# Kernel tuning notes

Measured on AMD Instinct MI355X. Metric: run time of the kernel, lower is better.

## Reference

```python
import jax, jax.numpy as jnp
import numpy as np

N = 100000       # nodes
E = 1600000      # edges (before self loops)
D = 128          # emb_dim
L = 5            # num_layer
NBOND = 62       # num_bond_type
NNODE = 2159     # num_node_type + 2
BN_EPS = 1e-5


def setup_inputs() -> dict:
    key = jax.random.key(0)
    ks = jax.random.split(key, 8)
    x = jax.random.randint(ks[0], (N, 1), 0, NNODE)
    edge_index = jax.random.randint(ks[1], (2, E), 0, N)
    edge_attr = jax.random.randint(ks[2], (E, 1), 0, NBOND)
    x_emb = jax.random.normal(ks[3], (NNODE, D), dtype=jnp.float32) * 0.02
    lin_w = jax.random.normal(ks[4], (L, D, D), dtype=jnp.float32) * (1.0 / np.sqrt(D))
    lin_b = jnp.zeros((L, D), jnp.float32)
    edge_tab = jax.random.normal(ks[5], (L, NBOND, D), dtype=jnp.float32) * 0.02
    bn_gamma = jnp.ones((L, D), jnp.float32)
    bn_beta = jnp.zeros((L, D), jnp.float32)
    return {"x": x, "edge_index": edge_index, "edge_attr": edge_attr,
            "x_emb": x_emb, "lin_w": lin_w, "lin_b": lin_b,
            "edge_tab": edge_tab, "bn_gamma": bn_gamma, "bn_beta": bn_beta}


def reference(x, edge_index, edge_attr, x_emb, lin_w, lin_b, edge_tab, bn_gamma, bn_beta):
    # node embedding lookup: x_embedding(x[:, 0])
    h = x_emb[x[:, 0]]                                  # [N, D]

    # add self loops (same for every layer in the torch code)
    loop = jnp.arange(N)
    src = jnp.concatenate([edge_index[0], loop])        # [E+N] = j (source)
    dst = jnp.concatenate([edge_index[1], loop])        # [E+N] = i (target)
    eids = jnp.concatenate([edge_attr[:, 0], jnp.zeros((N,), edge_attr.dtype)])

    # GCN symmetric norm: deg from row (=src), deg_inv_sqrt[row]*deg_inv_sqrt[col]
    deg = jax.ops.segment_sum(jnp.ones(src.shape, h.dtype), src, num_segments=N)
    dinv = jnp.where(deg > 0, jax.lax.rsqrt(deg), jnp.zeros_like(deg))
    norm = (dinv[src] * dinv[dst])[:, None]             # [E+N, 1]

    for l in range(L):
        # linear transform of nodes
        hl = h @ lin_w[l].T + lin_b[l]                  # [N, D]
        # message: norm * (x_j + edge_embedding), gather from source nodes
        msg = norm * (hl[src] + edge_tab[l][eids])      # [E+N, D]
        # aggr='add': scatter_add into target nodes
        agg = jax.ops.segment_sum(msg, dst, num_segments=N)  # [N, D]
        # BatchNorm1d (training-mode batch statistics, biased variance)
        mean = agg.mean(axis=0)
        var = jnp.mean((agg - mean) ** 2, axis=0)
        h = (agg - mean) * jax.lax.rsqrt(var + BN_EPS) * bn_gamma[l] + bn_beta[l]
        if l < L - 1:
            h = jax.nn.relu(h)
        # dropout with drop_ratio=0 is identity
    # JK == 'last'
    return h
```

## Files before the change

### kernel.cpp

```cpp
#include <hip/hip_runtime.h>

#define NN 100000
#define NE 1600000
#define NT (NE + NN)
#define DD 128
#define NL 5
#define NB 62
#define BN_EPS 1e-5f
#define NBUCK 391
#define PSUMNB 6250
#define RED1 128

typedef unsigned short ushort_t;
typedef unsigned int uint_t;
typedef short bf8 __attribute__((ext_vector_type(8)));
typedef float f32x4 __attribute__((ext_vector_type(4)));

static __device__ __forceinline__ float4 ld4(const float* p) { return *(const float4*)p; }

static __device__ __forceinline__ float bfhi(uint_t u) {
    uint_t x = u & 0xFFFF0000u;
    return __builtin_bit_cast(float, x);
}
static __device__ __forceinline__ float bflo(uint_t u) {
    uint_t x = u << 16;
    return __builtin_bit_cast(float, x);
}
static __device__ __forceinline__ ushort_t f2bf(float f) {
    uint_t u = __builtin_bit_cast(uint_t, f);
    u += 0x7FFFu + ((u >> 16) & 1u);
    return (ushort_t)(u >> 16);
}


__global__ void k_init(int* gbh_d, int* gbh_s, float* scale, float* shift,
                       int* row_ptr) {
    int i = blockIdx.x * 256 + threadIdx.x;
    if (i < NBUCK) { gbh_d[i] = 0; gbh_s[i] = 0; }
    if (i < DD) { scale[i] = 1.f; shift[i] = 0.f; }
    if (i == 0) row_ptr[NN] = NT;
}

__global__ void k_cvt(const float* __restrict__ src, ushort_t* __restrict__ dst,
                      int total) {
    int i = blockIdx.x * 256 + threadIdx.x;
    if (i < total) dst[i] = f2bf(src[i]);
}

__global__ __launch_bounds__(256) void k_binhist(const int* __restrict__ ei,
                                                 int* __restrict__ gbh_d,
                                                 int* __restrict__ gbh_s) {
    __shared__ int hd[NBUCK], hs[NBUCK];
    int tid = threadIdx.x;
    for (int b = tid; b < NBUCK; b += 256) { hd[b] = 0; hs[b] = 0; }
    __syncthreads();
    for (int idx = blockIdx.x * 256 + tid; idx < NT; idx += gridDim.x * 256) {
        int d = (idx < NE) ? ei[NE + idx] : idx - NE;
        atomicAdd(&hd[d >> 8], 1);
        if (idx < NE) atomicAdd(&hs[ei[idx] >> 8], 1);
    }
    __syncthreads();
    for (int b = tid; b < NBUCK; b += 256) {
        if (hd[b]) atomicAdd(&gbh_d[b], hd[b]);
        if (hs[b]) atomicAdd(&gbh_s[b], hs[b]);
    }
}

__global__ void k_scan391(const int* __restrict__ gbh_d, const int* __restrict__ gbh_s,
                          int* __restrict__ bb_d, int* __restrict__ cur_d,
                          int* __restrict__ bb_s, int* __restrict__ cur_s) {
    __shared__ int s[512];
    const int* g = blockIdx.x ? gbh_s : gbh_d;
    int* bb = blockIdx.x ? bb_s : bb_d;
    int* cur = blockIdx.x ? cur_s : cur_d;
    int t = threadIdx.x;
    int v = (t < NBUCK) ? g[t] : 0;
    s[t] = v;
    __syncthreads();
    for (int off = 1; off < 512; off <<= 1) {
        int val = (t >= off) ? s[t - off] : 0;
        __syncthreads();
        s[t] += val;
        __syncthreads();
    }
    if (t < NBUCK) { int e = s[t] - v; bb[t] = e; cur[t] = e; }
    if (t == 511) bb[NBUCK] = s[511];
}

#define CHUNK 4096
__global__ __launch_bounds__(256) void k_scat2(const int* __restrict__ ei,
                                               const int* __restrict__ ea,
                                               int* __restrict__ cur_d,
                                               int* __restrict__ cur_s,
                                               uint_t* __restrict__ rec_d,
                                               int* __restrict__ rec_s) {
    __shared__ int lhd[NBUCK], lbd[NBUCK], lhs[NBUCK], lbs[NBUCK];
    int tid = threadIdx.x;
    for (int b = tid; b < NBUCK; b += 256) { lhd[b] = 0; lhs[b] = 0; }
    __syncthreads();
    int base = blockIdx.x * CHUNK;
    uint_t rd[16];
    int rs[16], bkd[16], bks[16];
#pragma unroll
    for (int k = 0; k < 16; ++k) {
        int idx = base + tid + k * 256;
        bkd[k] = -1; bks[k] = -1;
        if (idx < NT) {
            int s, d, eid;
            if (idx < NE) {
                s = ei[idx]; d = ei[NE + idx]; eid = ea[idx];
                bks[k] = s >> 8; rs[k] = s;
                atomicAdd(&lhs[bks[k]], 1);
            } else {
                s = d = idx - NE; eid = 0;
            }
            bkd[k] = d >> 8;
            rd[k] = (uint_t)s | ((uint_t)eid << 17) | ((uint_t)(d & 255) << 24);
            atomicAdd(&lhd[bkd[k]], 1);
        }
    }
    __syncthreads();
    for (int b = tid; b < NBUCK; b += 256) {
        if (lhd[b]) lbd[b] = atomicAdd(&cur_d[b], lhd[b]);
        if (lhs[b]) lbs[b] = atomicAdd(&cur_s[b], lhs[b]);
    }
    __syncthreads();
    for (int b = tid; b < NBUCK; b += 256) { lhd[b] = 0; lhs[b] = 0; }
    __syncthreads();
#pragma unroll
    for (int k = 0; k < 16; ++k) {
        if (bkd[k] >= 0) {
            int rk = atomicAdd(&lhd[bkd[k]], 1);
            rec_d[lbd[bkd[k]] + rk] = rd[k];
        }
        if (bks[k] >= 0) {
            int rk = atomicAdd(&lhs[bks[k]], 1);
            rec_s[lbs[bks[k]] + rk] = rs[k];
        }
    }
}

__global__ __launch_bounds__(256) void k_srcfin(const int* __restrict__ rec,
                                                const int* __restrict__ bb,
                                                float* __restrict__ dinv) {
    __shared__ int h[256];
    int tid = threadIdx.x;
    h[tid] = 0;
    __syncthreads();
    int lo = bb[blockIdx.x], hi = bb[blockIdx.x + 1];
    for (int i = lo + tid; i < hi; i += 256) atomicAdd(&h[rec[i] & 255], 1);
    __syncthreads();
    int v = blockIdx.x * 256 + tid;
    if (v < NN) dinv[v] = rsqrtf((float)(h[tid] + 1));
}

__global__ __launch_bounds__(256) void k_dstfin(const uint_t* __restrict__ rec,
                                                const int* __restrict__ bb,
                                                const float* __restrict__ dinv,
                                                int* __restrict__ row_ptr,
                                                int* __restrict__ s_pack,
                                                float* __restrict__ s_norm) {
    __shared__ int h[256], sc[256], rpE[256];
    int tid = threadIdx.x;
    h[tid] = 0;
    __syncthreads();
    int lo = bb[blockIdx.x], hi = bb[blockIdx.x + 1];
    for (int i = lo + tid; i < hi; i += 256) atomicAdd(&h[(rec[i] >> 24) & 255], 1);
    __syncthreads();
    sc[tid] = h[tid];
    __syncthreads();
    for (int off = 1; off < 256; off <<= 1) {
        int val = (tid >= off) ? sc[tid - off] : 0;
        __syncthreads();
        sc[tid] += val;
        __syncthreads();
    }
    rpE[tid] = sc[tid] - h[tid];
    int v = blockIdx.x * 256 + tid;
    if (v < NN) row_ptr[v] = lo + rpE[tid];
    h[tid] = 0;
    __syncthreads();
    for (int i = lo + tid; i < hi; i += 256) {
        uint_t u = rec[i];
        int dl = (u >> 24) & 255;
        int rk = atomicAdd(&h[dl], 1);
        int slot = lo + rpE[dl] + rk;
        int s = u & 0x1FFFF;
        int e = (u >> 17) & 0x3F;
        s_pack[slot] = s | (e << 20);
        s_norm[slot] = dinv[s] * dinv[(blockIdx.x << 8) + dl];
    }
}

__global__ void k_h0b(const int* __restrict__ x, const float* __restrict__ emb,
                      ushort_t* __restrict__ Xb, int n) {
    int v = blockIdx.x * 16 + (threadIdx.x >> 4);
    if (v >= n) return;
    int c8 = (threadIdx.x & 15) * 8;
    const float* src = &emb[x[v] * DD + c8];
    uint_t pk[4];
#pragma unroll
    for (int j = 0; j < 4; ++j)
        pk[j] = (uint_t)f2bf(src[2 * j]) | ((uint_t)f2bf(src[2 * j + 1]) << 16);
    *(uint4*)&Xb[(size_t)v * DD + c8] = make_uint4(pk[0], pk[1], pk[2], pk[3]);
}


__global__ __launch_bounds__(256, 2) void k_gemm(const ushort_t* __restrict__ Xb,
                                                 const ushort_t* __restrict__ Wb,
                                                 const float* __restrict__ bias,
                                                 const float* __restrict__ scale,
                                                 const float* __restrict__ shift,
                                                 ushort_t* __restrict__ C,
                                                 int n, int relu) {
    __shared__ ushort_t As[128 * DD];
    __shared__ ushort_t Bs[128 * DD];
    const int tid = threadIdx.x;
    const int r0 = blockIdx.x * 128;
    const int rl = tid >> 4;
    const int kg = tid & 15;

    float sc[8], sh[8];
    *(float4*)&sc[0] = ld4(&scale[kg * 8]);
    *(float4*)&sc[4] = ld4(&scale[kg * 8 + 4]);
    *(float4*)&sh[0] = ld4(&shift[kg * 8]);
    *(float4*)&sh[4] = ld4(&shift[kg * 8 + 4]);

#pragma unroll
    for (int it = 0; it < 8; ++it) {
        int row = rl + it * 16;
        int grow = r0 + row;
        uint4 v = make_uint4(0, 0, 0, 0);
        if (grow < n) v = *(const uint4*)&Xb[(size_t)grow * DD + kg * 8];
        uint_t pk[4];
        const uint_t* pv = (const uint_t*)&v;
#pragma unroll
        for (int j = 0; j < 4; ++j) {
            float lo = fmaf(bflo(pv[j]), sc[2 * j], sh[2 * j]);
            float hi = fmaf(bfhi(pv[j]), sc[2 * j + 1], sh[2 * j + 1]);
            if (relu) { lo = fmaxf(lo, 0.f); hi = fmaxf(hi, 0.f); }
            pk[j] = (uint_t)f2bf(lo) | ((uint_t)f2bf(hi) << 16);
        }
        *(uint4*)&As[row * DD + (kg ^ (row & 7)) * 8] = make_uint4(pk[0], pk[1], pk[2], pk[3]);
        uint4 wv = *(const uint4*)&Wb[row * DD + kg * 8];
        *(uint4*)&Bs[row * DD + (kg ^ (row & 7)) * 8] = wv;
    }
    __syncthreads();

    const int w = tid >> 6;
    const int lane = tid & 63;
    const int lr = lane & 15;
    const int lg = lane >> 4;

    f32x4 acc[2][8];
#pragma unroll
    for (int rf = 0; rf < 2; ++rf)
#pragma unroll
        for (int cf = 0; cf < 8; ++cf)
#pragma unroll
            for (int r = 0; r < 4; ++r) acc[rf][cf][r] = 0.f;

#pragma unroll
    for (int ks = 0; ks < 4; ++ks) {
        int kgg = ks * 4 + lg;
        bf8 a0, a1;
        {
            int row = w * 32 + lr;
            a0 = *(bf8*)&As[row * DD + (kgg ^ (row & 7)) * 8];
            row += 16;
            a1 = *(bf8*)&As[row * DD + (kgg ^ (row & 7)) * 8];
        }
#pragma unroll
        for (int cf = 0; cf < 8; ++cf) {
            int col = cf * 16 + lr;
            bf8 b = *(bf8*)&Bs[col * DD + (kgg ^ (col & 7)) * 8];
            acc[0][cf] = __builtin_amdgcn_mfma_f32_16x16x32_bf16(a0, b, acc[0][cf], 0, 0, 0);
            acc[1][cf] = __builtin_amdgcn_mfma_f32_16x16x32_bf16(a1, b, acc[1][cf], 0, 0, 0);
        }
    }

#pragma unroll
    for (int cf = 0; cf < 8; ++cf) {
        int col = cf * 16 + lr;
        float bi = bias[col];
#pragma unroll
        for (int rf = 0; rf < 2; ++rf) {
#pragma unroll
            for (int r = 0; r < 4; ++r) {
                int grow = r0 + w * 32 + rf * 16 + lg * 4 + r;
                if (grow < n) C[(size_t)grow * DD + col] = f2bf(acc[rf][cf][r] + bi);
            }
        }
    }
}

__global__ __launch_bounds__(1024) void k_agg(const ushort_t* __restrict__ hl,
                                              const ushort_t* __restrict__ etab,
                                              const int* __restrict__ row_ptr,
                                              const int* __restrict__ s_pack,
                                              const float* __restrict__ s_norm,
                                              ushort_t* __restrict__ aggb,
                                              float* __restrict__ psumA,
                                              float* __restrict__ psumB, int n) {
    __shared__ float lsA[16][DD], lsB[16][DD];
    int tid = threadIdx.x;
    int wv = tid >> 6;
    int lane = tid & 63;
    int g = lane >> 4;
    int fl = lane & 15;
    int lane8 = fl * 8;
    int v = blockIdx.x * 16 + wv;
    int p0 = row_ptr[v], p1 = row_ptr[v + 1];

    float acc[8];
#pragma unroll
    for (int j = 0; j < 8; ++j) acc[j] = 0.f;
    for (int p = p0 + g; p < p1; p += 4) {
        int c = s_pack[p];
        float nr = s_norm[p];
        int s = c & 0xFFFFF;
        int e = c >> 20;
        uint4 hv = *(const uint4*)&hl[(size_t)s * DD + lane8];
        uint4 ev = *(const uint4*)&etab[e * DD + lane8];
        acc[0] = fmaf(nr, bflo(hv.x) + bflo(ev.x), acc[0]);
        acc[1] = fmaf(nr, bfhi(hv.x) + bfhi(ev.x), acc[1]);
        acc[2] = fmaf(nr, bflo(hv.y) + bflo(ev.y), acc[2]);
        acc[3] = fmaf(nr, bfhi(hv.y) + bfhi(ev.y), acc[3]);
        acc[4] = fmaf(nr, bflo(hv.z) + bflo(ev.z), acc[4]);
        acc[5] = fmaf(nr, bfhi(hv.z) + bfhi(ev.z), acc[5]);
        acc[6] = fmaf(nr, bflo(hv.w) + bflo(ev.w), acc[6]);
        acc[7] = fmaf(nr, bfhi(hv.w) + bfhi(ev.w), acc[7]);
    }
#pragma unroll
    for (int j = 0; j < 8; ++j) {
        acc[j] += __shfl_xor(acc[j], 16);
        acc[j] += __shfl_xor(acc[j], 32);
    }
    if (g == 0) {
        uint_t pk[4];
#pragma unroll
        for (int j = 0; j < 4; ++j)
            pk[j] = (uint_t)f2bf(acc[2 * j]) | ((uint_t)f2bf(acc[2 * j + 1]) << 16);
        *(uint4*)&aggb[(size_t)v * DD + lane8] = make_uint4(pk[0], pk[1], pk[2], pk[3]);
#pragma unroll
        for (int j = 0; j < 8; ++j) {
            lsA[wv][lane8 + j] = acc[j];
            lsB[wv][lane8 + j] = acc[j] * acc[j];
        }
    }
    __syncthreads();
    if (tid < DD) {
        float a = 0.f, b = 0.f;
#pragma unroll
        for (int k = 0; k < 16; ++k) { a += lsA[k][tid]; b += lsB[k][tid]; }
        psumA[(size_t)blockIdx.x * DD + tid] = a;
        psumB[(size_t)blockIdx.x * DD + tid] = b;
    }
}

__global__ __launch_bounds__(256) void k_bnred(const float* __restrict__ psumA,
                                               const float* __restrict__ psumB,
                                               float* __restrict__ partA,
                                               float* __restrict__ partB) {
    __shared__ float sa[2][DD], sb[2][DD];
    int d = threadIdx.x & 127;
    int half = threadIdx.x >> 7;
    float a = 0.f, b = 0.f;
    int iend = min(blockIdx.x * 49 + 49, PSUMNB);
    for (int i = blockIdx.x * 49 + half; i < iend; i += 2) {
        a += psumA[(size_t)i * DD + d];
        b += psumB[(size_t)i * DD + d];
    }
    sa[half][d] = a; sb[half][d] = b;
    __syncthreads();
    if (threadIdx.x < DD) {
        partA[blockIdx.x * DD + d] = sa[0][d] + sa[1][d];
        partB[blockIdx.x * DD + d] = sb[0][d] + sb[1][d];
    }
}

__global__ __launch_bounds__(256) void k_bnfin(const float* __restrict__ partA,
                                               const float* __restrict__ partB,
                                               const float* __restrict__ gamma,
                                               const float* __restrict__ beta,
                                               float* __restrict__ scale,
                                               float* __restrict__ shift, int n) {
    __shared__ float sa[2][DD], sb[2][DD];
    int d = threadIdx.x & 127;
    int half = threadIdx.x >> 7;
    float a = 0.f, b = 0.f;
    for (int i = half; i < RED1; i += 2) {
        a += partA[i * DD + d];
        b += partB[i * DD + d];
    }
    sa[half][d] = a; sb[half][d] = b;
    __syncthreads();
    if (threadIdx.x < DD) {
        float s = sa[0][d] + sa[1][d];
        float ss = sb[0][d] + sb[1][d];
        float mean = s / (float)n;
        float var = ss / (float)n - mean * mean;
        float sc = gamma[d] * rsqrtf(var + BN_EPS);
        scale[d] = sc;
        shift[d] = beta[d] - mean * sc;
    }
}

__global__ void k_bnapply(const ushort_t* __restrict__ Xb, float* __restrict__ out,
                          const float* __restrict__ scale,
                          const float* __restrict__ shift, int total8) {
    int i = blockIdx.x * blockDim.x + threadIdx.x;
    int stride = gridDim.x * blockDim.x;
    for (; i < total8; i += stride) {
        int c8 = (i & 15) * 8;
        uint4 v = *(const uint4*)&Xb[(size_t)i * 8];
        float4 sc0 = ld4(&scale[c8]), sc1 = ld4(&scale[c8 + 4]);
        float4 sh0 = ld4(&shift[c8]), sh1 = ld4(&shift[c8 + 4]);
        float4 o0, o1;
        o0.x = fmaf(bflo(v.x), sc0.x, sh0.x);
        o0.y = fmaf(bfhi(v.x), sc0.y, sh0.y);
        o0.z = fmaf(bflo(v.y), sc0.z, sh0.z);
        o0.w = fmaf(bfhi(v.y), sc0.w, sh0.w);
        o1.x = fmaf(bflo(v.z), sc1.x, sh1.x);
        o1.y = fmaf(bfhi(v.z), sc1.y, sh1.y);
        o1.z = fmaf(bflo(v.w), sc1.z, sh1.z);
        o1.w = fmaf(bfhi(v.w), sc1.w, sh1.w);
        *(float4*)&out[(size_t)i * 8] = o0;
        *(float4*)&out[(size_t)i * 8 + 4] = o1;
    }
}


extern "C" void kernel_launch(void* const* d_in, const int* in_sizes, int n_in,
                              void* d_out, int out_size, void* d_ws, size_t ws_size,
                              hipStream_t stream) {
    const int* x        = (const int*)d_in[0];
    const int* ei       = (const int*)d_in[1];
    const int* ea       = (const int*)d_in[2];
    const float* x_emb  = (const float*)d_in[3];
    const float* lin_w  = (const float*)d_in[4];
    const float* lin_b  = (const float*)d_in[5];
    const float* etab   = (const float*)d_in[6];
    const float* gamma  = (const float*)d_in[7];
    const float* beta   = (const float*)d_in[8];
    float* OUT = (float*)d_out;

    char* w = (char*)d_ws;
    size_t off = 0;
    auto alloc = [&](size_t bytes) -> void* {
        off = (off + 255) & ~(size_t)255;
        void* p = w + off;
        off += bytes;
        return p;
    };
    ushort_t* Xb     = (ushort_t*)alloc((size_t)NN * DD * 2);
    ushort_t* hl     = (ushort_t*)alloc((size_t)NN * DD * 2);
    ushort_t* etabb  = (ushort_t*)alloc((size_t)NL * NB * DD * 2);
    ushort_t* Wb     = (ushort_t*)alloc((size_t)NL * DD * DD * 2);
    uint_t* rec_d    = (uint_t*)alloc((size_t)NT * 4);
    int*    rec_s    = (int*)alloc((size_t)NE * 4);
    int*   s_pack    = (int*)alloc((size_t)NT * 4);
    float* s_norm    = (float*)alloc((size_t)NT * 4);
    int*   rowp      = (int*)alloc((size_t)(NN + 1) * 4);
    float* dinv      = (float*)alloc((size_t)NN * 4);
    int*   gbh_d     = (int*)alloc((size_t)NBUCK * 4);
    int*   gbh_s     = (int*)alloc((size_t)NBUCK * 4);
    int*   bb_d      = (int*)alloc((size_t)(NBUCK + 1) * 4);
    int*   bb_s      = (int*)alloc((size_t)(NBUCK + 1) * 4);
    int*   cur_d     = (int*)alloc((size_t)NBUCK * 4);
    int*   cur_s     = (int*)alloc((size_t)NBUCK * 4);
    float* psumA     = (float*)alloc((size_t)DD * PSUMNB * 4);
    float* psumB     = (float*)alloc((size_t)DD * PSUMNB * 4);
    float* partA     = (float*)alloc((size_t)DD * RED1 * 4);
    float* partB     = (float*)alloc((size_t)DD * RED1 * 4);
    float* scale     = (float*)alloc((size_t)DD * 4);
    float* shift     = (float*)alloc((size_t)DD * 4);

    const int etabTot = NL * NB * DD;
    const int wTot = NL * DD * DD;

    k_init<<<(NN + 255) / 256, 256, 0, stream>>>(gbh_d, gbh_s, scale, shift, rowp);
    k_cvt<<<(etabTot + 255) / 256, 256, 0, stream>>>(etab, etabb, etabTot);
    k_cvt<<<(wTot + 255) / 256, 256, 0, stream>>>(lin_w, Wb, wTot);
    k_binhist<<<256, 256, 0, stream>>>(ei, gbh_d, gbh_s);
    k_scan391<<<2, 512, 0, stream>>>(gbh_d, gbh_s, bb_d, cur_d, bb_s, cur_s);
    k_scat2<<<(NT + CHUNK - 1) / CHUNK, 256, 0, stream>>>(ei, ea, cur_d, cur_s,
                                                          rec_d, rec_s);
    k_srcfin<<<NBUCK, 256, 0, stream>>>(rec_s, bb_s, dinv);
    k_dstfin<<<NBUCK, 256, 0, stream>>>(rec_d, bb_d, dinv, rowp, s_pack, s_norm);
    k_h0b<<<(NN + 15) / 16, 256, 0, stream>>>(x, x_emb, Xb, NN);

    for (int l = 0; l < NL; ++l) {
        k_gemm<<<(NN + 127) / 128, 256, 0, stream>>>(Xb, Wb + (size_t)l * DD * DD,
                                                     lin_b + (size_t)l * DD,
                                                     scale, shift, hl, NN, l > 0 ? 1 : 0);
        k_agg<<<PSUMNB, 1024, 0, stream>>>(hl, etabb + (size_t)l * NB * DD,
                                           rowp, s_pack, s_norm, Xb, psumA, psumB, NN);
        k_bnred<<<RED1, 256, 0, stream>>>(psumA, psumB, partA, partB);
        k_bnfin<<<1, 256, 0, stream>>>(partA, partB, gamma + (size_t)l * DD,
                                       beta + (size_t)l * DD, scale, shift, NN);
    }
    k_bnapply<<<(NN * DD / 8 + 255) / 256, 256, 0, stream>>>(Xb, OUT, scale, shift,
                                                             NN * DD / 8);
}
```

Baseline: 816.1 us.

## Map one 16-lane group per node in aggregation with 4-way unrolled gathers

```diff
diff --git a/kernel.cpp b/kernel.cpp
--- a/kernel.cpp
+++ b/kernel.cpp
@@ -30,6 +30,17 @@
     uint_t u = __builtin_bit_cast(uint_t, f);
     u += 0x7FFFu + ((u >> 16) & 1u);
     return (ushort_t)(u >> 16);
+}
+
+static __device__ __forceinline__ void accum8(float* acc, uint4 hv, uint4 ev, float nr) {
+    acc[0] = fmaf(nr, bflo(hv.x) + bflo(ev.x), acc[0]);
+    acc[1] = fmaf(nr, bfhi(hv.x) + bfhi(ev.x), acc[1]);
+    acc[2] = fmaf(nr, bflo(hv.y) + bflo(ev.y), acc[2]);
+    acc[3] = fmaf(nr, bfhi(hv.y) + bfhi(ev.y), acc[3]);
+    acc[4] = fmaf(nr, bflo(hv.z) + bflo(ev.z), acc[4]);
+    acc[5] = fmaf(nr, bfhi(hv.z) + bfhi(ev.z), acc[5]);
+    acc[6] = fmaf(nr, bflo(hv.w) + bflo(ev.w), acc[6]);
+    acc[7] = fmaf(nr, bfhi(hv.w) + bfhi(ev.w), acc[7]);
 }
 
 
@@ -294,67 +305,81 @@
     }
 }
 
-__global__ __launch_bounds__(1024) void k_agg(const ushort_t* __restrict__ hl,
-                                              const ushort_t* __restrict__ etab,
-                                              const int* __restrict__ row_ptr,
-                                              const int* __restrict__ s_pack,
-                                              const float* __restrict__ s_norm,
-                                              ushort_t* __restrict__ aggb,
-                                              float* __restrict__ psumA,
-                                              float* __restrict__ psumB, int n) {
-    __shared__ float lsA[16][DD], lsB[16][DD];
+__global__ __launch_bounds__(256) void k_agg(const ushort_t* __restrict__ hl,
+                                             const ushort_t* __restrict__ etab,
+                                             const int* __restrict__ row_ptr,
+                                             const int* __restrict__ s_pack,
+                                             const float* __restrict__ s_norm,
+                                             ushort_t* __restrict__ aggb,
+                                             float* __restrict__ psumA,
+                                             float* __restrict__ psumB, int n) {
+    __shared__ float lsA[4][DD], lsB[4][DD];
     int tid = threadIdx.x;
+
+    int v = blockIdx.x * 16 + (tid >> 4);
+    int lane8 = (tid & 15) * 8;
+    int p0 = row_ptr[v], p1 = row_ptr[v + 1];
+    float acc[8];
+#pragma unroll
+    for (int j = 0; j < 8; ++j) acc[j] = 0.f;
+
+    int p = p0;
+    for (; p + 4 <= p1; p += 4) {
+        int c0 = s_pack[p], c1 = s_pack[p + 1], c2 = s_pack[p + 2], c3 = s_pack[p + 3];
+        float n0 = s_norm[p], n1 = s_norm[p + 1], n2 = s_norm[p + 2], n3 = s_norm[p + 3];
+        uint4 h0 = *(const uint4*)&hl[(size_t)(c0 & 0xFFFFF) * DD + lane8];
+        uint4 h1 = *(const uint4*)&hl[(size_t)(c1 & 0xFFFFF) * DD + lane8];
+        uint4 h2 = *(const uint4*)&hl[(size_t)(c2 & 0xFFFFF) * DD + lane8];
+        uint4 h3 = *(const uint4*)&hl[(size_t)(c3 & 0xFFFFF) * DD + lane8];
+        uint4 e0 = *(const uint4*)&etab[(c0 >> 20) * DD + lane8];
+        uint4 e1 = *(const uint4*)&etab[(c1 >> 20) * DD + lane8];
+        uint4 e2 = *(const uint4*)&etab[(c2 >> 20) * DD + lane8];
+        uint4 e3 = *(const uint4*)&etab[(c3 >> 20) * DD + lane8];
+        accum8(acc, h0, e0, n0);
+        accum8(acc, h1, e1, n1);
+        accum8(acc, h2, e2, n2);
+        accum8(acc, h3, e3, n3);
+    }
+    for (; p < p1; ++p) {
+        int c = s_pack[p];
+        float nr = s_norm[p];
+        uint4 hv = *(const uint4*)&hl[(size_t)(c & 0xFFFFF) * DD + lane8];
+        uint4 ev = *(const uint4*)&etab[(c >> 20) * DD + lane8];
+        accum8(acc, hv, ev, nr);
+    }
+
+    uint_t pk[4];
+#pragma unroll
+    for (int j = 0; j < 4; ++j)
+        pk[j] = (uint_t)f2bf(acc[2 * j]) | ((uint_t)f2bf(acc[2 * j + 1]) << 16);
+    *(uint4*)&aggb[(size_t)v * DD + lane8] = make_uint4(pk[0], pk[1], pk[2], pk[3]);
+
+    float s0[8], s1[8];
+#pragma unroll
+    for (int j = 0; j < 8; ++j) { s0[j] = acc[j]; s1[j] = acc[j] * acc[j]; }
+#pragma unroll
+    for (int m = 16; m <= 32; m <<= 1) {
+#pragma unroll
+        for (int j = 0; j < 8; ++j) {
+            s0[j] += __shfl_xor(s0[j], m);
+            s1[j] += __shfl_xor(s1[j], m);
+        }
+    }
     int wv = tid >> 6;
     int lane = tid & 63;
-    int g = lane >> 4;
-    int fl = lane & 15;
-    int lane8 = fl * 8;
-    int v = blockIdx.x * 16 + wv;
-    int p0 = row_ptr[v], p1 = row_ptr[v + 1];
-
-    float acc[8];
-#pragma unroll
-    for (int j = 0; j < 8; ++j) acc[j] = 0.f;
-    for (int p = p0 + g; p < p1; p += 4) {
-        int c = s_pack[p];
-        float nr = s_norm[p];
-        int s = c & 0xFFFFF;
-        int e = c >> 20;
-        uint4 hv = *(const uint4*)&hl[(size_t)s * DD + lane8];
-        uint4 ev = *(const uint4*)&etab[e * DD + lane8];
-        acc[0] = fmaf(nr, bflo(hv.x) + bflo(ev.x), acc[0]);
-        acc[1] = fmaf(nr, bfhi(hv.x) + bfhi(ev.x), acc[1]);
-        acc[2] = fmaf(nr, bflo(hv.y) + bflo(ev.y), acc[2]);
-        acc[3] = fmaf(nr, bfhi(hv.y) + bfhi(ev.y), acc[3]);
-        acc[4] = fmaf(nr, bflo(hv.z) + bflo(ev.z), acc[4]);
-        acc[5] = fmaf(nr, bfhi(hv.z) + bfhi(ev.z), acc[5]);
-        acc[6] = fmaf(nr, bflo(hv.w) + bflo(ev.w), acc[6]);
-        acc[7] = fmaf(nr, bfhi(hv.w) + bfhi(ev.w), acc[7]);
-    }
-#pragma unroll
-    for (int j = 0; j < 8; ++j) {
-        acc[j] += __shfl_xor(acc[j], 16);
-        acc[j] += __shfl_xor(acc[j], 32);
-    }
-    if (g == 0) {
-        uint_t pk[4];
-#pragma unroll
-        for (int j = 0; j < 4; ++j)
-            pk[j] = (uint_t)f2bf(acc[2 * j]) | ((uint_t)f2bf(acc[2 * j + 1]) << 16);
-        *(uint4*)&aggb[(size_t)v * DD + lane8] = make_uint4(pk[0], pk[1], pk[2], pk[3]);
+    if (lane < 16) {
 #pragma unroll
         for (int j = 0; j < 8; ++j) {
-            lsA[wv][lane8 + j] = acc[j];
-            lsB[wv][lane8 + j] = acc[j] * acc[j];
+            lsA[wv][lane8 + j] = s0[j];
+            lsB[wv][lane8 + j] = s1[j];
         }
     }
     __syncthreads();
     if (tid < DD) {
-        float a = 0.f, b = 0.f;
-#pragma unroll
-        for (int k = 0; k < 16; ++k) { a += lsA[k][tid]; b += lsB[k][tid]; }
-        psumA[(size_t)blockIdx.x * DD + tid] = a;
-        psumB[(size_t)blockIdx.x * DD + tid] = b;
+        psumA[(size_t)blockIdx.x * DD + tid] =
+            lsA[0][tid] + lsA[1][tid] + lsA[2][tid] + lsA[3][tid];
+        psumB[(size_t)blockIdx.x * DD + tid] =
+            lsB[0][tid] + lsB[1][tid] + lsB[2][tid] + lsB[3][tid];
     }
 }
 
@@ -494,8 +519,8 @@
         k_gemm<<<(NN + 127) / 128, 256, 0, stream>>>(Xb, Wb + (size_t)l * DD * DD,
                                                      lin_b + (size_t)l * DD,
                                                      scale, shift, hl, NN, l > 0 ? 1 : 0);
-        k_agg<<<PSUMNB, 1024, 0, stream>>>(hl, etabb + (size_t)l * NB * DD,
-                                           rowp, s_pack, s_norm, Xb, psumA, psumB, NN);
+        k_agg<<<PSUMNB, 256, 0, stream>>>(hl, etabb + (size_t)l * NB * DD,
+                                          rowp, s_pack, s_norm, Xb, psumA, psumB, NN);
         k_bnred<<<RED1, 256, 0, stream>>>(psumA, psumB, partA, partB);
         k_bnfin<<<1, 256, 0, stream>>>(partA, partB, gamma + (size_t)l * DD,
                                        beta + (size_t)l * DD, scale, shift, NN);
```

Measured after the change: 733.3 us. 1.11x faster.
